# Kernel tuning notes

Hardware: AMD Instinct MI355X
Metric: run time of the kernel (lower is better)

The kernel has to match this reference:

```python
import jax, jax.numpy as jnp
import numpy as np
from jax import lax

# Model dims (match init_kwargs / input_specs)
B, L, DIN, H = 8, 2048, 40, 128
NL, DSTATE, DCONV, EXPAND, DTRANK = 4, 16, 4, 2, 8
DINNER = EXPAND * H
NHOR, NCLS = 3, 3


def _layer_norm(x, g, b, eps=1e-5):
    m = jnp.mean(x, -1, keepdims=True)
    v = jnp.mean((x - m) ** 2, -1, keepdims=True)
    return (x - m) * lax.rsqrt(v + eps) * g + b


def _mamba_block(x, in_w, cw, cb, xp_w, dt_w, dt_b, A_log, Dp, out_w):
    # x: (b, l, H)
    b, l, _ = x.shape
    xz = x @ in_w.T                      # (b, l, 2*d_inner)
    xh, z = jnp.split(xz, 2, axis=-1)
    # causal depthwise conv1d (torch pads d_conv-1 both sides then slices [:l])
    xc = lax.conv_general_dilated(
        xh.transpose(0, 2, 1), cw, window_strides=(1,),
        padding=[(DCONV - 1, 0)], feature_group_count=DINNER,
        dimension_numbers=('NCH', 'OIH', 'NCH')) + cb[None, :, None]
    xh = jax.nn.silu(xc.transpose(0, 2, 1))   # (b, l, d_inner)
    # selective SSM
    A = -jnp.exp(A_log)                   # (N,)
    xp = xh @ xp_w.T                      # (b, l, dt_rank + 2N)
    dt_in, Bm, Cm = jnp.split(xp, [DTRANK, DTRANK + DSTATE], axis=-1)
    delta = jax.nn.softplus(dt_in @ dt_w.T + dt_b)          # (b, l, d_inner)
    dA = jnp.exp(delta[..., None] * A)                      # (b, l, d_inner, N)
    dBx = delta[..., None] * Bm[:, :, None, :] * xh[..., None]

    def step(h, inp):
        dA_t, dBx_t, C_t = inp
        h = dA_t * h + dBx_t              # (b, d_inner, N)
        y = jnp.einsum('bdn,bn->bd', h, C_t)
        return h, y

    h0 = jnp.zeros((b, DINNER, DSTATE), x.dtype)
    _, ys = lax.scan(step, h0, (dA.transpose(1, 0, 2, 3),
                                dBx.transpose(1, 0, 2, 3),
                                Cm.transpose(1, 0, 2)))
    y = ys.transpose(1, 0, 2) + Dp * xh   # (b, l, d_inner)
    y = y * jax.nn.silu(z)
    return y @ out_w.T                    # (b, l, H)


def _forward(x, input_proj_w, input_proj_b, input_norm_g, input_norm_b,
             norm_g, norm_b, in_proj_w, conv_w, conv_b, x_proj_w,
             dt_proj_w, dt_proj_b, A_log, D, out_proj_w,
             head_w1, head_b1, head_w2, head_b2):
    h = _layer_norm(x @ input_proj_w.T + input_proj_b, input_norm_g, input_norm_b)
    for i in range(NL):  # residual Mamba blocks (pre-norm)
        h = h + _mamba_block(_layer_norm(h, norm_g[i], norm_b[i]),
                             in_proj_w[i], conv_w[i], conv_b[i], x_proj_w[i],
                             dt_proj_w[i], dt_proj_b[i], A_log[i], D[i], out_proj_w[i])
    feats = h[:, -1, :]                   # last-timestep features (b, H)
    logits = []
    for i in range(NHOR):
        t = jax.nn.gelu(feats @ head_w1[i].T + head_b1[i], approximate=False)
        logits.append(t @ head_w2[i].T + head_b2[i])
    return jnp.stack(logits, axis=1)      # (b, num_horizons, num_classes)


def setup_inputs() -> dict:
    key = jax.random.key(0)
    ks = jax.random.split(key, 12)
    rn = lambda k, s, sc=0.02: jax.random.normal(k, s, jnp.float32) * sc
    A0 = jnp.log(jnp.arange(1, DSTATE + 1, dtype=jnp.float32))
    return {
        'x': jax.random.normal(ks[0], (B, L, DIN), jnp.float32),
        'input_proj_w': rn(ks[1], (H, DIN)),
        'input_proj_b': jnp.zeros((H,), jnp.float32),
        'input_norm_g': jnp.ones((H,), jnp.float32),
        'input_norm_b': jnp.zeros((H,), jnp.float32),
        'norm_g': jnp.ones((NL, H), jnp.float32),
        'norm_b': jnp.zeros((NL, H), jnp.float32),
        'in_proj_w': rn(ks[2], (NL, 2 * DINNER, H)),
        'conv_w': rn(ks[3], (NL, DINNER, 1, DCONV), 0.1),
        'conv_b': jnp.zeros((NL, DINNER), jnp.float32),
        'x_proj_w': rn(ks[4], (NL, DTRANK + 2 * DSTATE, DINNER)),
        'dt_proj_w': rn(ks[5], (NL, DINNER, DTRANK), 0.1),
        'dt_proj_b': rn(ks[6], (NL, DINNER), 0.1),
        'A_log': jnp.tile(A0, (NL, 1)),
        'D': jnp.ones((NL, DINNER), jnp.float32),
        'out_proj_w': rn(ks[7], (NL, H, DINNER)),
        'head_w1': rn(ks[8], (NHOR, H // 2, H)),
        'head_b1': jnp.zeros((NHOR, H // 2), jnp.float32),
        'head_w2': rn(ks[9], (NHOR, NCLS, H // 2)),
        'head_b2': jnp.zeros((NHOR, NCLS), jnp.float32),
    }


def reference(x, input_proj_w, input_proj_b, input_norm_g, input_norm_b,
              norm_g, norm_b, in_proj_w, conv_w, conv_b, x_proj_w,
              dt_proj_w, dt_proj_b, A_log, D, out_proj_w,
              head_w1, head_b1, head_w2, head_b2):
    return _forward(x, input_proj_w, input_proj_b, input_norm_g, input_norm_b,
                    norm_g, norm_b, in_proj_w, conv_w, conv_b, x_proj_w,
                    dt_proj_w, dt_proj_b, A_log, D, out_proj_w,
                    head_w1, head_b1, head_w2, head_b2)
```

## Files before the change

kernel.cpp:

```cpp
#include <hip/hip_runtime.h>
#include <hip/hip_bf16.h>
#include <math.h>

#define B_  8
#define L_  2048
#define DIN_ 40
#define H_  128
#define NL_ 4
#define DSTATE_ 16
#define DCONV_ 4
#define DTRANK_ 8
#define DINNER_ 256
#define NHOR_ 3
#define NCLS_ 3

#define CL_ 16
#define NC_ 128

__device__ __forceinline__ float softplus_f(float x) {
  return fmaxf(x, 0.f) + log1pf(__expf(-fabsf(x)));
}

__device__ __forceinline__ bool a_is_arith(const float* Ag, float& An0) {
  An0 = -__expf(Ag[0]);
  if (An0 == 0.f) return false;
  bool ok = true;
#pragma unroll
  for (int n = 1; n < DSTATE_; n++) {
    float r = -__expf(Ag[n]) / An0;
    ok = ok && (fabsf(r - (float)(n + 1)) < 1e-3f);
  }
  return ok;
}

__global__ __launch_bounds__(128) void k_in_ln(
    const float* __restrict__ x, const float* __restrict__ w,
    const float* __restrict__ bias, const float* __restrict__ g,
    const float* __restrict__ bb, float* __restrict__ hout)
{
  int row = blockIdx.x;
  int o = threadIdx.x;
  __shared__ float xs[DIN_];
  __shared__ float sm[4];
  if (o < DIN_) xs[o] = x[(size_t)row * DIN_ + o];
  __syncthreads();
  float acc = bias[o];
  const float* wr = w + (size_t)o * DIN_;
#pragma unroll
  for (int k = 0; k < DIN_; k++) acc += xs[k] * wr[k];
  float s = acc;
#pragma unroll
  for (int m = 32; m >= 1; m >>= 1) s += __shfl_xor(s, m);
  if ((o & 63) == 0) sm[o >> 6] = s;
  __syncthreads();
  float mean = (sm[0] + sm[1]) * (1.f / H_);
  float dv = acc - mean;
  float q = dv * dv;
#pragma unroll
  for (int m = 32; m >= 1; m >>= 1) q += __shfl_xor(q, m);
  if ((o & 63) == 0) sm[2 + (o >> 6)] = q;
  __syncthreads();
  float var = (sm[2] + sm[3]) * (1.f / H_);
  hout[(size_t)row * H_ + o] = dv * rsqrtf(var + 1e-5f) * g[o] + bb[o];
}

__global__ __launch_bounds__(128) void k_ln(
    const float* __restrict__ in, const float* __restrict__ g,
    const float* __restrict__ bb, float* __restrict__ out)
{
  int row = blockIdx.x;
  int o = threadIdx.x;
  float v = in[(size_t)row * H_ + o];
  __shared__ float sm[4];
  float s = v;
#pragma unroll
  for (int m = 32; m >= 1; m >>= 1) s += __shfl_xor(s, m);
  if ((o & 63) == 0) sm[o >> 6] = s;
  __syncthreads();
  float mean = (sm[0] + sm[1]) * (1.f / H_);
  float dv = v - mean;
  float q = dv * dv;
#pragma unroll
  for (int m = 32; m >= 1; m >>= 1) q += __shfl_xor(q, m);
  if ((o & 63) == 0) sm[2 + (o >> 6)] = q;
  __syncthreads();
  float var = (sm[2] + sm[3]) * (1.f / H_);
  out[(size_t)row * H_ + o] = dv * rsqrtf(var + 1e-5f) * g[o] + bb[o];
}

template <int BM, int BN, int EPI>
__global__ __launch_bounds__(256) void gemm_tn(
    const float* __restrict__ A, const float* __restrict__ Bw,
    float* __restrict__ C0, float* __restrict__ C1,
    int M, int N, int K)
{
  constexpr int TM = BM / 16, TN = BN / 16;
  __shared__ float As[16][BM + 4];
  __shared__ float Bs[16][BN + 4];
  const int tid = threadIdx.x;
  const int tx = tid & 15, ty = tid >> 4;
  const int bm0 = blockIdx.y * BM, bn0 = blockIdx.x * BN;
  float acc[TM][TN] = {};
  constexpr int AF4 = BM / 64;
  constexpr int BF4 = BN / 64;

  for (int k0 = 0; k0 < K; k0 += 16) {
#pragma unroll
    for (int i = 0; i < AF4; i++) {
      int f = tid + i * 256;
      int r = f >> 2, kq = (f & 3) << 2;
      float4 v = *reinterpret_cast<const float4*>(&A[(size_t)(bm0 + r) * K + k0 + kq]);
      As[kq + 0][r] = v.x; As[kq + 1][r] = v.y;
      As[kq + 2][r] = v.z; As[kq + 3][r] = v.w;
    }
#pragma unroll
    for (int i = 0; i < BF4; i++) {
      int f = tid + i * 256;
      int rn = f >> 2, kq = (f & 3) << 2;
      float4 v = make_float4(0.f, 0.f, 0.f, 0.f);
      if (bn0 + rn < N)
        v = *reinterpret_cast<const float4*>(&Bw[(size_t)(bn0 + rn) * K + k0 + kq]);
      Bs[kq + 0][rn] = v.x; Bs[kq + 1][rn] = v.y;
      Bs[kq + 2][rn] = v.z; Bs[kq + 3][rn] = v.w;
    }
    __syncthreads();
#pragma unroll
    for (int k = 0; k < 16; k++) {
      float a[TM], b[TN];
#pragma unroll
      for (int i = 0; i < TM; i += 4) {
        float4 v = *reinterpret_cast<const float4*>(&As[k][ty * TM + i]);
        a[i] = v.x; a[i + 1] = v.y; a[i + 2] = v.z; a[i + 3] = v.w;
      }
#pragma unroll
      for (int j = 0; j < TN; j += 4) {
        float4 v = *reinterpret_cast<const float4*>(&Bs[k][tx * TN + j]);
        b[j] = v.x; b[j + 1] = v.y; b[j + 2] = v.z; b[j + 3] = v.w;
      }
#pragma unroll
      for (int i = 0; i < TM; i++)
#pragma unroll
        for (int j = 0; j < TN; j++) acc[i][j] += a[i] * b[j];
    }
    __syncthreads();
  }

#pragma unroll
  for (int i = 0; i < TM; i++) {
    int r = bm0 + ty * TM + i;
    int c0 = bn0 + tx * TN;
    if (c0 >= N) continue;
    float4 v = make_float4(acc[i][0], acc[i][1], acc[i][2], acc[i][3]);
    if (EPI == 0) {
      *reinterpret_cast<float4*>(&C0[(size_t)r * N + c0]) = v;
    } else {
      if (c0 < 256) *reinterpret_cast<float4*>(&C0[(size_t)r * 256 + c0]) = v;
      else          *reinterpret_cast<float4*>(&C1[(size_t)r * 256 + (c0 - 256)]) = v;
    }
  }
}

template <bool DO_LN>
__global__ __launch_bounds__(256) void gemm_out(
    const float* __restrict__ A, const float* __restrict__ Bw,
    float* __restrict__ H, float* __restrict__ XN,
    const float* __restrict__ g, const float* __restrict__ bb)
{
  constexpr int BM = 64, BN = 128, K = DINNER_, N = H_;
  constexpr int TM = 4, TN = 8;
  __shared__ float As[16][BM + 4];
  __shared__ float Bs[16][BN + 4];
  const int tid = threadIdx.x;
  const int tx = tid & 15, ty = tid >> 4;
  const int bm0 = blockIdx.x * BM;
  float acc[TM][TN] = {};

  for (int k0 = 0; k0 < K; k0 += 16) {
    {
      int f = tid;
      int r = f >> 2, kq = (f & 3) << 2;
      float4 v = *reinterpret_cast<const float4*>(&A[(size_t)(bm0 + r) * K + k0 + kq]);
      As[kq + 0][r] = v.x; As[kq + 1][r] = v.y;
      As[kq + 2][r] = v.z; As[kq + 3][r] = v.w;
    }
#pragma unroll
    for (int i = 0; i < 2; i++) {
      int f = tid + i * 256;
      int rn = f >> 2, kq = (f & 3) << 2;
      float4 v = *reinterpret_cast<const float4*>(&Bw[(size_t)rn * K + k0 + kq]);
      Bs[kq + 0][rn] = v.x; Bs[kq + 1][rn] = v.y;
      Bs[kq + 2][rn] = v.z; Bs[kq + 3][rn] = v.w;
    }
    __syncthreads();
#pragma unroll
    for (int k = 0; k < 16; k++) {
      float a[TM], b[TN];
      float4 av = *reinterpret_cast<const float4*>(&As[k][ty * TM]);
      a[0] = av.x; a[1] = av.y; a[2] = av.z; a[3] = av.w;
#pragma unroll
      for (int j = 0; j < TN; j += 4) {
        float4 v = *reinterpret_cast<const float4*>(&Bs[k][tx * TN + j]);
        b[j] = v.x; b[j + 1] = v.y; b[j + 2] = v.z; b[j + 3] = v.w;
      }
#pragma unroll
      for (int i = 0; i < TM; i++)
#pragma unroll
        for (int j = 0; j < TN; j++) acc[i][j] += a[i] * b[j];
    }
    __syncthreads();
  }

  float gv[TN], bv[TN];
  if (DO_LN) {
#pragma unroll
    for (int j = 0; j < TN; j += 4) {
      float4 t = *reinterpret_cast<const float4*>(&g[tx * TN + j]);
      gv[j] = t.x; gv[j+1] = t.y; gv[j+2] = t.z; gv[j+3] = t.w;
      float4 u = *reinterpret_cast<const float4*>(&bb[tx * TN + j]);
      bv[j] = u.x; bv[j+1] = u.y; bv[j+2] = u.z; bv[j+3] = u.w;
    }
  }
#pragma unroll
  for (int i = 0; i < TM; i++) {
    int r = bm0 + ty * TM + i;
    float hv[TN];
#pragma unroll
    for (int j = 0; j < TN; j += 4) {
      float4 o = *reinterpret_cast<const float4*>(&H[(size_t)r * N + tx * TN + j]);
      hv[j]   = o.x + acc[i][j];
      hv[j+1] = o.y + acc[i][j+1];
      hv[j+2] = o.z + acc[i][j+2];
      hv[j+3] = o.w + acc[i][j+3];
    }
#pragma unroll
    for (int j = 0; j < TN; j += 4)
      *reinterpret_cast<float4*>(&H[(size_t)r * N + tx * TN + j]) =
          make_float4(hv[j], hv[j+1], hv[j+2], hv[j+3]);
    if (DO_LN) {
      float s = 0.f;
#pragma unroll
      for (int j = 0; j < TN; j++) s += hv[j];
#pragma unroll
      for (int m = 1; m < 16; m <<= 1) s += __shfl_xor(s, m);
      float mean = s * (1.f / N);
      float q = 0.f;
#pragma unroll
      for (int j = 0; j < TN; j++) { float d = hv[j] - mean; q += d * d; }
#pragma unroll
      for (int m = 1; m < 16; m <<= 1) q += __shfl_xor(q, m);
      float rstd = rsqrtf(q * (1.f / N) + 1e-5f);
      float xo[TN];
#pragma unroll
      for (int j = 0; j < TN; j++) xo[j] = (hv[j] - mean) * rstd * gv[j] + bv[j];
#pragma unroll
      for (int j = 0; j < TN; j += 4)
        *reinterpret_cast<float4*>(&XN[(size_t)r * N + tx * TN + j]) =
            make_float4(xo[j], xo[j+1], xo[j+2], xo[j+3]);
    }
  }
}

__global__ __launch_bounds__(256) void k_conv(
    const float* __restrict__ xx, const float* __restrict__ cw,
    const float* __restrict__ cb, float* __restrict__ xh)
{
  int idx = blockIdx.x * 256 + threadIdx.x;
  int d = idx & 255;
  int bt = idx >> 8;
  int t = bt & (L_ - 1);
  float acc = cb[d];
#pragma unroll
  for (int k = 0; k < DCONV_; k++) {
    int ts = t - 3 + k;
    if (ts >= 0) acc += cw[d * DCONV_ + k] * xx[(size_t)(bt - 3 + k) * 256 + d];
  }
  xh[idx] = acc / (1.f + __expf(-acc));
}

__global__ __launch_bounds__(256, 4) void k_scan1(
    const float* __restrict__ xh, const float* __restrict__ xp,
    const float* __restrict__ dtw, const float* __restrict__ dtb,
    const float* __restrict__ Ag,
    float* __restrict__ hf, float* __restrict__ ss)
{
  int b = blockIdx.x >> 7;
  int c = blockIdx.x & (NC_ - 1);
  int d = threadIdx.x;
  __shared__ float xps[CL_][40];
  {
    const float* xrow = xp + ((size_t)b * L_ + c * CL_) * 40;
    for (int i = threadIdx.x; i < CL_ * 40; i += 256) xps[i / 40][i % 40] = xrow[i];
  }
  float dtw_r[DTRANK_];
#pragma unroll
  for (int k = 0; k < DTRANK_; k++) dtw_r[k] = dtw[d * DTRANK_ + k];
  float dtb_r = dtb[d];
  float An0;
  bool fast = a_is_arith(Ag, An0);
  __syncthreads();
  float h[DSTATE_] = {};
  float S = 0.f;
  size_t base = ((size_t)b * L_ + c * CL_) * 256 + d;
  if (fast) {
#pragma unroll
    for (int tt = 0; tt < CL_; tt++) {
      float acc = dtb_r;
#pragma unroll
      for (int k = 0; k < DTRANK_; k++) acc += xps[tt][k] * dtw_r[k];
      float dv = softplus_f(acc);
      float xv = xh[base + tt * 256];
      S += dv;
      float dx = dv * xv;
      float E = __expf(dv * An0);
      float f = E;
#pragma unroll
      for (int n = 0; n < DSTATE_; n++) {
        h[n] = f * h[n] + dx * xps[tt][8 + n];
        f *= E;
      }
    }
  } else {
    for (int tt = 0; tt < CL_; tt++) {
      float acc = dtb_r;
#pragma unroll
      for (int k = 0; k < DTRANK_; k++) acc += xps[tt][k] * dtw_r[k];
      float dv = softplus_f(acc);
      float xv = xh[base + tt * 256];
      S += dv;
      float dx = dv * xv;
      for (int n = 0; n < DSTATE_; n++) {
        float dA = __expf(dv * (-__expf(Ag[n])));
        h[n] = dA * h[n] + dx * xps[tt][8 + n];
      }
    }
  }
  ss[(size_t)blockIdx.x * 256 + d] = S;
  float* hp = hf + ((size_t)blockIdx.x * 256 + d) * DSTATE_;
#pragma unroll
  for (int n = 0; n < DSTATE_; n += 4)
    *reinterpret_cast<float4*>(&hp[n]) = make_float4(h[n], h[n+1], h[n+2], h[n+3]);
}

__global__ __launch_bounds__(64) void k_scan2(
    const float* __restrict__ Ag, const float* __restrict__ ss,
    float* __restrict__ hf)
{
  int gid = blockIdx.x * 64 + threadIdx.x;
  int b = gid >> 12;
  int r = gid & 4095;
  int d = r >> 4;
  int n = r & 15;
  float An = -__expf(Ag[n]);
  float hi = 0.f;
  for (int ct = 0; ct < NC_ / 8; ct++) {
    float f[8], s[8];
#pragma unroll
    for (int j = 0; j < 8; j++) {
      int c = ct * 8 + j;
      f[j] = hf[((size_t)(b * NC_ + c) * 4096) + r];
      s[j] = ss[(size_t)(b * NC_ + c) * 256 + d];
    }
#pragma unroll
    for (int j = 0; j < 8; j++) {
      int c = ct * 8 + j;
      float P = __expf(An * s[j]);
      hf[((size_t)(b * NC_ + c) * 4096) + r] = hi;
      hi = P * hi + f[j];
    }
  }
}

__global__ __launch_bounds__(256, 4) void k_scan3(
    const float* __restrict__ xh, const float* __restrict__ xp,
    const float* __restrict__ dtw, const float* __restrict__ dtb,
    const float* __restrict__ Ag, const float* __restrict__ hf,
    const float* __restrict__ Dp, float* zy)
{
  int b = blockIdx.x >> 7;
  int c = blockIdx.x & (NC_ - 1);
  int d = threadIdx.x;
  __shared__ float xps[CL_][40];
  {
    const float* xrow = xp + ((size_t)b * L_ + c * CL_) * 40;
    for (int i = threadIdx.x; i < CL_ * 40; i += 256) xps[i / 40][i % 40] = xrow[i];
  }
  float dtw_r[DTRANK_];
#pragma unroll
  for (int k = 0; k < DTRANK_; k++) dtw_r[k] = dtw[d * DTRANK_ + k];
  float dtb_r = dtb[d];
  float An0;
  bool fast = a_is_arith(Ag, An0);
  __syncthreads();
  float h[DSTATE_];
  {
    const float* hp = hf + ((size_t)blockIdx.x * 256 + d) * DSTATE_;
#pragma unroll
    for (int n = 0; n < DSTATE_; n += 4) {
      float4 v = *reinterpret_cast<const float4*>(&hp[n]);
      h[n] = v.x; h[n+1] = v.y; h[n+2] = v.z; h[n+3] = v.w;
    }
  }
  float Dv = Dp[d];
  size_t base = ((size_t)b * L_ + c * CL_) * 256 + d;
  if (fast) {
#pragma unroll
    for (int tt = 0; tt < CL_; tt++) {
      float acc = dtb_r;
#pragma unroll
      for (int k = 0; k < DTRANK_; k++) acc += xps[tt][k] * dtw_r[k];
      float dv = softplus_f(acc);
      float xv = xh[base + tt * 256];
      float dx = dv * xv;
      float E = __expf(dv * An0);
      float f = E;
      float y = 0.f;
#pragma unroll
      for (int n = 0; n < DSTATE_; n++) {
        h[n] = f * h[n] + dx * xps[tt][8 + n];
        y += h[n] * xps[tt][24 + n];
        f *= E;
      }
      float yv = y + Dv * xv;
      float zv = zy[base + tt * 256];
      zy[base + tt * 256] = yv * (zv / (1.f + __expf(-zv)));
    }
  } else {
    for (int tt = 0; tt < CL_; tt++) {
      float acc = dtb_r;
#pragma unroll
      for (int k = 0; k < DTRANK_; k++) acc += xps[tt][k] * dtw_r[k];
      float dv = softplus_f(acc);
      float xv = xh[base + tt * 256];
      float dx = dv * xv;
      float y = 0.f;
      for (int n = 0; n < DSTATE_; n++) {
        float dA = __expf(dv * (-__expf(Ag[n])));
        h[n] = dA * h[n] + dx * xps[tt][8 + n];
        y += h[n] * xps[tt][24 + n];
      }
      float yv = y + Dv * xv;
      float zv = zy[base + tt * 256];
      zy[base + tt * 256] = yv * (zv / (1.f + __expf(-zv)));
    }
  }
}

__global__ __launch_bounds__(64) void k_heads(
    const float* __restrict__ hbuf, const float* __restrict__ w1,
    const float* __restrict__ b1, const float* __restrict__ w2,
    const float* __restrict__ b2, float* __restrict__ out)
{
  int hor = blockIdx.x, b = blockIdx.y;
  int j = threadIdx.x;
  __shared__ float fs[H_];
  __shared__ float ts[64];
  const float* fr = hbuf + ((size_t)b * L_ + (L_ - 1)) * H_;
  fs[j] = fr[j];
  fs[j + 64] = fr[j + 64];
  __syncthreads();
  float acc = b1[hor * 64 + j];
  const float* wr = w1 + (size_t)(hor * 64 + j) * H_;
#pragma unroll
  for (int k = 0; k < H_; k++) acc += fs[k] * wr[k];
  ts[j] = 0.5f * acc * (1.f + erff(acc * 0.70710678118654752f));
  __syncthreads();
  if (j < NCLS_) {
    float a2 = b2[hor * NCLS_ + j];
    const float* w2r = w2 + (size_t)(hor * NCLS_ + j) * 64;
    float s = a2;
#pragma unroll
    for (int k = 0; k < 64; k++) s += ts[k] * w2r[k];
    out[(size_t)b * (NHOR_ * NCLS_) + hor * NCLS_ + j] = s;
  }
}

extern "C" void kernel_launch(void* const* d_in, const int* in_sizes, int n_in,
                              void* d_out, int out_size, void* d_ws, size_t ws_size,
                              hipStream_t stream)
{
  const float* x            = (const float*)d_in[0];
  const float* input_proj_w = (const float*)d_in[1];
  const float* input_proj_b = (const float*)d_in[2];
  const float* input_norm_g = (const float*)d_in[3];
  const float* input_norm_b = (const float*)d_in[4];
  const float* norm_g       = (const float*)d_in[5];
  const float* norm_b       = (const float*)d_in[6];
  const float* in_proj_w    = (const float*)d_in[7];
  const float* conv_w       = (const float*)d_in[8];
  const float* conv_b       = (const float*)d_in[9];
  const float* x_proj_w     = (const float*)d_in[10];
  const float* dt_proj_w    = (const float*)d_in[11];
  const float* dt_proj_b    = (const float*)d_in[12];
  const float* A_log        = (const float*)d_in[13];
  const float* Dp           = (const float*)d_in[14];
  const float* out_proj_w   = (const float*)d_in[15];
  const float* head_w1      = (const float*)d_in[16];
  const float* head_b1      = (const float*)d_in[17];
  const float* head_w2      = (const float*)d_in[18];
  const float* head_b2      = (const float*)d_in[19];
  float* out = (float*)d_out;

  const int ROWS = B_ * L_;
  float* ws = (float*)d_ws;
  float* h    = ws;
  float* xn   = h  + (size_t)ROWS * H_;
  float* xx   = xn + (size_t)ROWS * H_;
  float* zz   = xx + (size_t)ROWS * 256;
  float* xh   = zz + (size_t)ROWS * 256;
  float* xp   = xh + (size_t)ROWS * 256;
  float* ss   = xp + (size_t)ROWS * 40;
  float* hf   = xx;

  k_in_ln<<<ROWS, 128, 0, stream>>>(x, input_proj_w, input_proj_b,
                                    input_norm_g, input_norm_b, h);
  k_ln<<<ROWS, 128, 0, stream>>>(h, norm_g, norm_b, xn);

  for (int l = 0; l < NL_; l++) {
    gemm_tn<128, 64, 2><<<dim3(512 / 64, ROWS / 128), 256, 0, stream>>>(
        xn, in_proj_w + (size_t)l * 512 * H_, xx, zz, ROWS, 512, H_);
    k_conv<<<ROWS, 256, 0, stream>>>(xx, conv_w + (size_t)l * DINNER_ * DCONV_,
                                     conv_b + (size_t)l * DINNER_, xh);
    gemm_tn<64, 64, 0><<<dim3(1, ROWS / 64), 256, 0, stream>>>(
        xh, x_proj_w + (size_t)l * 40 * DINNER_, xp, nullptr, ROWS, 40, DINNER_);
    k_scan1<<<B_ * NC_, 256, 0, stream>>>(xh, xp,
        dt_proj_w + (size_t)l * DINNER_ * DTRANK_, dt_proj_b + (size_t)l * DINNER_,
        A_log + l * DSTATE_, hf, ss);
    k_scan2<<<(B_ * DINNER_ * DSTATE_) / 64, 64, 0, stream>>>(A_log + l * DSTATE_, ss, hf);
    k_scan3<<<B_ * NC_, 256, 0, stream>>>(xh, xp,
        dt_proj_w + (size_t)l * DINNER_ * DTRANK_, dt_proj_b + (size_t)l * DINNER_,
        A_log + l * DSTATE_, hf, Dp + (size_t)l * DINNER_, zz);
    if (l < NL_ - 1) {
      gemm_out<true><<<ROWS / 64, 256, 0, stream>>>(
          zz, out_proj_w + (size_t)l * H_ * DINNER_, h, xn,
          norm_g + (l + 1) * H_, norm_b + (l + 1) * H_);
    } else {
      gemm_out<false><<<ROWS / 64, 256, 0, stream>>>(
          zz, out_proj_w + (size_t)l * H_ * DINNER_, h, nullptr, nullptr, nullptr);
    }
  }

  k_heads<<<dim3(NHOR_, B_), 64, 0, stream>>>(h, head_w1, head_b1, head_w2, head_b2, out);
}
```

Before: 831.9 us.

## Fuse conv, x_proj and chunk scan; correct chunk outputs from carried state

```diff
diff --git a/kernel.cpp b/kernel.cpp
--- a/kernel.cpp
+++ b/kernel.cpp
@@ -14,8 +14,8 @@
 #define NHOR_ 3
 #define NCLS_ 3
 
-#define CL_ 16
-#define NC_ 128
+#define CL_ 32
+#define NC_ 64
 
 __device__ __forceinline__ float softplus_f(float x) {
   return fmaxf(x, 0.f) + log1pf(__expf(-fabsf(x)));
@@ -260,78 +260,98 @@
   }
 }
 
-__global__ __launch_bounds__(256) void k_conv(
+__global__ __launch_bounds__(256, 4) void k_front(
     const float* __restrict__ xx, const float* __restrict__ cw,
-    const float* __restrict__ cb, float* __restrict__ xh)
-{
-  int idx = blockIdx.x * 256 + threadIdx.x;
-  int d = idx & 255;
-  int bt = idx >> 8;
-  int t = bt & (L_ - 1);
-  float acc = cb[d];
-#pragma unroll
-  for (int k = 0; k < DCONV_; k++) {
-    int ts = t - 3 + k;
-    if (ts >= 0) acc += cw[d * DCONV_ + k] * xx[(size_t)(bt - 3 + k) * 256 + d];
-  }
-  xh[idx] = acc / (1.f + __expf(-acc));
-}
-
-__global__ __launch_bounds__(256, 4) void k_scan1(
-    const float* __restrict__ xh, const float* __restrict__ xp,
+    const float* __restrict__ cb, const float* __restrict__ xpw,
     const float* __restrict__ dtw, const float* __restrict__ dtb,
-    const float* __restrict__ Ag,
+    const float* __restrict__ Ag, const float* __restrict__ Dp,
+    float* __restrict__ xpg, float* __restrict__ ylbuf,
     float* __restrict__ hf, float* __restrict__ ss)
 {
-  int b = blockIdx.x >> 7;
+  int b = blockIdx.x >> 6;
   int c = blockIdx.x & (NC_ - 1);
   int d = threadIdx.x;
-  __shared__ float xps[CL_][40];
-  {
-    const float* xrow = xp + ((size_t)b * L_ + c * CL_) * 40;
-    for (int i = threadIdx.x; i < CL_ * 40; i += 256) xps[i / 40][i % 40] = xrow[i];
-  }
+  int row0 = b * L_ + c * CL_;
+
+  __shared__ float xhs[CL_][256];
+  __shared__ float xps[CL_ * 40];
+
+  float w0 = cw[d * DCONV_ + 0], w1 = cw[d * DCONV_ + 1];
+  float w2 = cw[d * DCONV_ + 2], w3 = cw[d * DCONV_ + 3];
+  float cbv = cb[d];
+  float xm3 = (c > 0) ? xx[(size_t)(row0 - 3) * 256 + d] : 0.f;
+  float xm2 = (c > 0) ? xx[(size_t)(row0 - 2) * 256 + d] : 0.f;
+  float xm1 = (c > 0) ? xx[(size_t)(row0 - 1) * 256 + d] : 0.f;
+#pragma unroll
+  for (int t = 0; t < CL_; t++) {
+    float xc = xx[(size_t)(row0 + t) * 256 + d];
+    float a = cbv + w0 * xm3 + w1 * xm2 + w2 * xm1 + w3 * xc;
+    xhs[t][d] = a / (1.f + __expf(-a));
+    xm3 = xm2; xm2 = xm1; xm1 = xc;
+  }
+  __syncthreads();
+
+  for (int o = d; o < CL_ * 40; o += 256) {
+    int t = o / 40, j = o - t * 40;
+    const float* wrow = xpw + (size_t)j * 256;
+    float av = 0.f;
+#pragma unroll
+    for (int k = 0; k < 256; k += 4) {
+      float4 wv = *reinterpret_cast<const float4*>(&wrow[k]);
+      float4 xv = *reinterpret_cast<const float4*>(&xhs[t][k]);
+      av += xv.x * wv.x + xv.y * wv.y + xv.z * wv.z + xv.w * wv.w;
+    }
+    xps[o] = av;
+    xpg[(size_t)row0 * 40 + o] = av;
+  }
+  __syncthreads();
+
   float dtw_r[DTRANK_];
 #pragma unroll
   for (int k = 0; k < DTRANK_; k++) dtw_r[k] = dtw[d * DTRANK_ + k];
   float dtb_r = dtb[d];
+  float Dv = Dp[d];
   float An0;
   bool fast = a_is_arith(Ag, An0);
-  __syncthreads();
   float h[DSTATE_] = {};
   float S = 0.f;
-  size_t base = ((size_t)b * L_ + c * CL_) * 256 + d;
+  size_t base = (size_t)row0 * 256 + d;
   if (fast) {
 #pragma unroll
-    for (int tt = 0; tt < CL_; tt++) {
+    for (int t = 0; t < CL_; t++) {
       float acc = dtb_r;
 #pragma unroll
-      for (int k = 0; k < DTRANK_; k++) acc += xps[tt][k] * dtw_r[k];
+      for (int k = 0; k < DTRANK_; k++) acc += xps[t * 40 + k] * dtw_r[k];
       float dv = softplus_f(acc);
-      float xv = xh[base + tt * 256];
+      float xv = xhs[t][d];
       S += dv;
       float dx = dv * xv;
       float E = __expf(dv * An0);
-      float f = E;
+      float f = E, y = 0.f;
 #pragma unroll
       for (int n = 0; n < DSTATE_; n++) {
-        h[n] = f * h[n] + dx * xps[tt][8 + n];
+        h[n] = f * h[n] + dx * xps[t * 40 + 8 + n];
+        y += h[n] * xps[t * 40 + 24 + n];
         f *= E;
       }
+      ylbuf[base + t * 256] = y + Dv * xv;
     }
   } else {
-    for (int tt = 0; tt < CL_; tt++) {
+    for (int t = 0; t < CL_; t++) {
       float acc = dtb_r;
 #pragma unroll
-      for (int k = 0; k < DTRANK_; k++) acc += xps[tt][k] * dtw_r[k];
+      for (int k = 0; k < DTRANK_; k++) acc += xps[t * 40 + k] * dtw_r[k];
       float dv = softplus_f(acc);
-      float xv = xh[base + tt * 256];
+      float xv = xhs[t][d];
       S += dv;
       float dx = dv * xv;
+      float y = 0.f;
       for (int n = 0; n < DSTATE_; n++) {
         float dA = __expf(dv * (-__expf(Ag[n])));
-        h[n] = dA * h[n] + dx * xps[tt][8 + n];
+        h[n] = dA * h[n] + dx * xps[t * 40 + 8 + n];
+        y += h[n] * xps[t * 40 + 24 + n];
       }
+      ylbuf[base + t * 256] = y + Dv * xv;
     }
   }
   ss[(size_t)blockIdx.x * 256 + d] = S;
@@ -371,19 +391,17 @@
 }
 
 __global__ __launch_bounds__(256, 4) void k_scan3(
-    const float* __restrict__ xh, const float* __restrict__ xp,
-    const float* __restrict__ dtw, const float* __restrict__ dtb,
-    const float* __restrict__ Ag, const float* __restrict__ hf,
-    const float* __restrict__ Dp, float* zy)
-{
-  int b = blockIdx.x >> 7;
+    const float* __restrict__ xpg, const float* __restrict__ dtw,
+    const float* __restrict__ dtb, const float* __restrict__ Ag,
+    const float* __restrict__ hf, const float* __restrict__ ylbuf,
+    float* zz)
+{
+  int b = blockIdx.x >> 6;
   int c = blockIdx.x & (NC_ - 1);
   int d = threadIdx.x;
-  __shared__ float xps[CL_][40];
-  {
-    const float* xrow = xp + ((size_t)b * L_ + c * CL_) * 40;
-    for (int i = threadIdx.x; i < CL_ * 40; i += 256) xps[i / 40][i % 40] = xrow[i];
-  }
+  int row0 = b * L_ + c * CL_;
+  __shared__ float xps[CL_ * 40];
+  for (int i = d; i < CL_ * 40; i += 256) xps[i] = xpg[(size_t)row0 * 40 + i];
   float dtw_r[DTRANK_];
 #pragma unroll
   for (int k = 0; k < DTRANK_; k++) dtw_r[k] = dtw[d * DTRANK_ + k];
@@ -391,56 +409,47 @@
   float An0;
   bool fast = a_is_arith(Ag, An0);
   __syncthreads();
-  float h[DSTATE_];
+  float h0[DSTATE_];
   {
     const float* hp = hf + ((size_t)blockIdx.x * 256 + d) * DSTATE_;
 #pragma unroll
     for (int n = 0; n < DSTATE_; n += 4) {
       float4 v = *reinterpret_cast<const float4*>(&hp[n]);
-      h[n] = v.x; h[n+1] = v.y; h[n+2] = v.z; h[n+3] = v.w;
-    }
-  }
-  float Dv = Dp[d];
-  size_t base = ((size_t)b * L_ + c * CL_) * 256 + d;
+      h0[n] = v.x; h0[n+1] = v.y; h0[n+2] = v.z; h0[n+3] = v.w;
+    }
+  }
+  size_t base = (size_t)row0 * 256 + d;
+  float cd = 0.f;
   if (fast) {
 #pragma unroll
-    for (int tt = 0; tt < CL_; tt++) {
+    for (int t = 0; t < CL_; t++) {
       float acc = dtb_r;
 #pragma unroll
-      for (int k = 0; k < DTRANK_; k++) acc += xps[tt][k] * dtw_r[k];
-      float dv = softplus_f(acc);
-      float xv = xh[base + tt * 256];
-      float dx = dv * xv;
-      float E = __expf(dv * An0);
-      float f = E;
-      float y = 0.f;
+      for (int k = 0; k < DTRANK_; k++) acc += xps[t * 40 + k] * dtw_r[k];
+      cd += softplus_f(acc);
+      float E = __expf(cd * An0);
+      float p = E, corr = 0.f;
 #pragma unroll
       for (int n = 0; n < DSTATE_; n++) {
-        h[n] = f * h[n] + dx * xps[tt][8 + n];
-        y += h[n] * xps[tt][24 + n];
-        f *= E;
+        corr += p * h0[n] * xps[t * 40 + 24 + n];
+        p *= E;
       }
-      float yv = y + Dv * xv;
-      float zv = zy[base + tt * 256];
-      zy[base + tt * 256] = yv * (zv / (1.f + __expf(-zv)));
+      float yv = ylbuf[base + t * 256] + corr;
+      float zv = zz[base + t * 256];
+      zz[base + t * 256] = yv * (zv / (1.f + __expf(-zv)));
     }
   } else {
-    for (int tt = 0; tt < CL_; tt++) {
+    for (int t = 0; t < CL_; t++) {
       float acc = dtb_r;
 #pragma unroll
-      for (int k = 0; k < DTRANK_; k++) acc += xps[tt][k] * dtw_r[k];
-      float dv = softplus_f(acc);
-      float xv = xh[base + tt * 256];
-      float dx = dv * xv;
-      float y = 0.f;
-      for (int n = 0; n < DSTATE_; n++) {
-        float dA = __expf(dv * (-__expf(Ag[n])));
-        h[n] = dA * h[n] + dx * xps[tt][8 + n];
-        y += h[n] * xps[tt][24 + n];
-      }
-      float yv = y + Dv * xv;
-      float zv = zy[base + tt * 256];
-      zy[base + tt * 256] = yv * (zv / (1.f + __expf(-zv)));
+      for (int k = 0; k < DTRANK_; k++) acc += xps[t * 40 + k] * dtw_r[k];
+      cd += softplus_f(acc);
+      float corr = 0.f;
+      for (int n = 0; n < DSTATE_; n++)
+        corr += __expf(cd * (-__expf(Ag[n]))) * h0[n] * xps[t * 40 + 24 + n];
+      float yv = ylbuf[base + t * 256] + corr;
+      float zv = zz[base + t * 256];
+      zz[base + t * 256] = yv * (zv / (1.f + __expf(-zv)));
     }
   }
 }
@@ -502,14 +511,14 @@
 
   const int ROWS = B_ * L_;
   float* ws = (float*)d_ws;
-  float* h    = ws;
-  float* xn   = h  + (size_t)ROWS * H_;
-  float* xx   = xn + (size_t)ROWS * H_;
-  float* zz   = xx + (size_t)ROWS * 256;
-  float* xh   = zz + (size_t)ROWS * 256;
-  float* xp   = xh + (size_t)ROWS * 256;
-  float* ss   = xp + (size_t)ROWS * 40;
-  float* hf   = xx;
+  float* h     = ws;
+  float* xn    = h  + (size_t)ROWS * H_;
+  float* xx    = xn + (size_t)ROWS * H_;
+  float* zz    = xx + (size_t)ROWS * 256;
+  float* ylbuf = zz + (size_t)ROWS * 256;
+  float* xp    = ylbuf + (size_t)ROWS * 256;
+  float* ss    = xp + (size_t)ROWS * 40;
+  float* hf    = xn;
 
   k_in_ln<<<ROWS, 128, 0, stream>>>(x, input_proj_w, input_proj_b,
                                     input_norm_g, input_norm_b, h);
@@ -518,17 +527,16 @@
   for (int l = 0; l < NL_; l++) {
     gemm_tn<128, 64, 2><<<dim3(512 / 64, ROWS / 128), 256, 0, stream>>>(
         xn, in_proj_w + (size_t)l * 512 * H_, xx, zz, ROWS, 512, H_);
-    k_conv<<<ROWS, 256, 0, stream>>>(xx, conv_w + (size_t)l * DINNER_ * DCONV_,
-                                     conv_b + (size_t)l * DINNER_, xh);
-    gemm_tn<64, 64, 0><<<dim3(1, ROWS / 64), 256, 0, stream>>>(
-        xh, x_proj_w + (size_t)l * 40 * DINNER_, xp, nullptr, ROWS, 40, DINNER_);
-    k_scan1<<<B_ * NC_, 256, 0, stream>>>(xh, xp,
+    k_front<<<B_ * NC_, 256, 0, stream>>>(
+        xx, conv_w + (size_t)l * DINNER_ * DCONV_, conv_b + (size_t)l * DINNER_,
+        x_proj_w + (size_t)l * 40 * DINNER_,
         dt_proj_w + (size_t)l * DINNER_ * DTRANK_, dt_proj_b + (size_t)l * DINNER_,
-        A_log + l * DSTATE_, hf, ss);
+        A_log + l * DSTATE_, Dp + (size_t)l * DINNER_,
+        xp, ylbuf, hf, ss);
     k_scan2<<<(B_ * DINNER_ * DSTATE_) / 64, 64, 0, stream>>>(A_log + l * DSTATE_, ss, hf);
-    k_scan3<<<B_ * NC_, 256, 0, stream>>>(xh, xp,
-        dt_proj_w + (size_t)l * DINNER_ * DTRANK_, dt_proj_b + (size_t)l * DINNER_,
-        A_log + l * DSTATE_, hf, Dp + (size_t)l * DINNER_, zz);
+    k_scan3<<<B_ * NC_, 256, 0, stream>>>(
+        xp, dt_proj_w + (size_t)l * DINNER_ * DTRANK_, dt_proj_b + (size_t)l * DINNER_,
+        A_log + l * DSTATE_, hf, ylbuf, zz);
     if (l < NL_ - 1) {
       gemm_out<true><<<ROWS / 64, 256, 0, stream>>>(
           zz, out_proj_w + (size_t)l * H_ * DINNER_, h, xn,
```

Result: slower. 933.8 us (+12.3%).

## Compute local scan outputs in pass one, apply carry-in correction in pass three

Applied to the files above, without the earlier changes.

```diff
diff --git a/kernel.cpp b/kernel.cpp
--- a/kernel.cpp
+++ b/kernel.cpp
@@ -148,14 +148,17 @@
 #pragma unroll
   for (int i = 0; i < TM; i++) {
     int r = bm0 + ty * TM + i;
-    int c0 = bn0 + tx * TN;
-    if (c0 >= N) continue;
-    float4 v = make_float4(acc[i][0], acc[i][1], acc[i][2], acc[i][3]);
-    if (EPI == 0) {
-      *reinterpret_cast<float4*>(&C0[(size_t)r * N + c0]) = v;
-    } else {
-      if (c0 < 256) *reinterpret_cast<float4*>(&C0[(size_t)r * 256 + c0]) = v;
-      else          *reinterpret_cast<float4*>(&C1[(size_t)r * 256 + (c0 - 256)]) = v;
+#pragma unroll
+    for (int jj = 0; jj < TN; jj += 4) {
+      int c0 = bn0 + tx * TN + jj;
+      if (c0 >= N) continue;
+      float4 v = make_float4(acc[i][jj], acc[i][jj+1], acc[i][jj+2], acc[i][jj+3]);
+      if (EPI == 0) {
+        *reinterpret_cast<float4*>(&C0[(size_t)r * N + c0]) = v;
+      } else {
+        if (c0 < 256) *reinterpret_cast<float4*>(&C0[(size_t)r * 256 + c0]) = v;
+        else          *reinterpret_cast<float4*>(&C1[(size_t)r * 256 + (c0 - 256)]) = v;
+      }
     }
   }
 }
@@ -277,10 +280,10 @@
   xh[idx] = acc / (1.f + __expf(-acc));
 }
 
-__global__ __launch_bounds__(256, 4) void k_scan1(
-    const float* __restrict__ xh, const float* __restrict__ xp,
+__global__ __launch_bounds__(256, 4) void k_scan1y(
+    float* xh_yl, const float* __restrict__ xp,
     const float* __restrict__ dtw, const float* __restrict__ dtb,
-    const float* __restrict__ Ag,
+    const float* __restrict__ Ag, const float* __restrict__ Dp,
     float* __restrict__ hf, float* __restrict__ ss)
 {
   int b = blockIdx.x >> 7;
@@ -295,6 +298,7 @@
 #pragma unroll
   for (int k = 0; k < DTRANK_; k++) dtw_r[k] = dtw[d * DTRANK_ + k];
   float dtb_r = dtb[d];
+  float Dv = Dp[d];
   float An0;
   bool fast = a_is_arith(Ag, An0);
   __syncthreads();
@@ -308,16 +312,18 @@
 #pragma unroll
       for (int k = 0; k < DTRANK_; k++) acc += xps[tt][k] * dtw_r[k];
       float dv = softplus_f(acc);
-      float xv = xh[base + tt * 256];
+      float xv = xh_yl[base + tt * 256];
       S += dv;
       float dx = dv * xv;
       float E = __expf(dv * An0);
-      float f = E;
+      float f = E, y = 0.f;
 #pragma unroll
       for (int n = 0; n < DSTATE_; n++) {
         h[n] = f * h[n] + dx * xps[tt][8 + n];
+        y += h[n] * xps[tt][24 + n];
         f *= E;
       }
+      xh_yl[base + tt * 256] = y + Dv * xv;
     }
   } else {
     for (int tt = 0; tt < CL_; tt++) {
@@ -325,13 +331,16 @@
 #pragma unroll
       for (int k = 0; k < DTRANK_; k++) acc += xps[tt][k] * dtw_r[k];
       float dv = softplus_f(acc);
-      float xv = xh[base + tt * 256];
+      float xv = xh_yl[base + tt * 256];
       S += dv;
       float dx = dv * xv;
+      float y = 0.f;
       for (int n = 0; n < DSTATE_; n++) {
         float dA = __expf(dv * (-__expf(Ag[n])));
         h[n] = dA * h[n] + dx * xps[tt][8 + n];
-      }
+        y += h[n] * xps[tt][24 + n];
+      }
+      xh_yl[base + tt * 256] = y + Dv * xv;
     }
   }
   ss[(size_t)blockIdx.x * 256 + d] = S;
@@ -370,20 +379,18 @@
   }
 }
 
-__global__ __launch_bounds__(256, 4) void k_scan3(
-    const float* __restrict__ xh, const float* __restrict__ xp,
-    const float* __restrict__ dtw, const float* __restrict__ dtb,
-    const float* __restrict__ Ag, const float* __restrict__ hf,
-    const float* __restrict__ Dp, float* zy)
+__global__ __launch_bounds__(256, 4) void k_scan3c(
+    const float* __restrict__ xpg, const float* __restrict__ dtw,
+    const float* __restrict__ dtb, const float* __restrict__ Ag,
+    const float* __restrict__ hf, const float* __restrict__ ylbuf,
+    float* zz)
 {
   int b = blockIdx.x >> 7;
   int c = blockIdx.x & (NC_ - 1);
   int d = threadIdx.x;
-  __shared__ float xps[CL_][40];
-  {
-    const float* xrow = xp + ((size_t)b * L_ + c * CL_) * 40;
-    for (int i = threadIdx.x; i < CL_ * 40; i += 256) xps[i / 40][i % 40] = xrow[i];
-  }
+  int row0 = b * L_ + c * CL_;
+  __shared__ float xps[CL_ * 40];
+  for (int i = d; i < CL_ * 40; i += 256) xps[i] = xpg[(size_t)row0 * 40 + i];
   float dtw_r[DTRANK_];
 #pragma unroll
   for (int k = 0; k < DTRANK_; k++) dtw_r[k] = dtw[d * DTRANK_ + k];
@@ -391,56 +398,47 @@
   float An0;
   bool fast = a_is_arith(Ag, An0);
   __syncthreads();
-  float h[DSTATE_];
+  float h0[DSTATE_];
   {
     const float* hp = hf + ((size_t)blockIdx.x * 256 + d) * DSTATE_;
 #pragma unroll
     for (int n = 0; n < DSTATE_; n += 4) {
       float4 v = *reinterpret_cast<const float4*>(&hp[n]);
-      h[n] = v.x; h[n+1] = v.y; h[n+2] = v.z; h[n+3] = v.w;
-    }
-  }
-  float Dv = Dp[d];
-  size_t base = ((size_t)b * L_ + c * CL_) * 256 + d;
+      h0[n] = v.x; h0[n+1] = v.y; h0[n+2] = v.z; h0[n+3] = v.w;
+    }
+  }
+  size_t base = (size_t)row0 * 256 + d;
+  float cd = 0.f;
   if (fast) {
 #pragma unroll
-    for (int tt = 0; tt < CL_; tt++) {
+    for (int t = 0; t < CL_; t++) {
       float acc = dtb_r;
 #pragma unroll
-      for (int k = 0; k < DTRANK_; k++) acc += xps[tt][k] * dtw_r[k];
-      float dv = softplus_f(acc);
-      float xv = xh[base + tt * 256];
-      float dx = dv * xv;
-      float E = __expf(dv * An0);
-      float f = E;
-      float y = 0.f;
+      for (int k = 0; k < DTRANK_; k++) acc += xps[t * 40 + k] * dtw_r[k];
+      cd += softplus_f(acc);
+      float E = __expf(cd * An0);
+      float p = E, corr = 0.f;
 #pragma unroll
       for (int n = 0; n < DSTATE_; n++) {
-        h[n] = f * h[n] + dx * xps[tt][8 + n];
-        y += h[n] * xps[tt][24 + n];
-        f *= E;
-      }
-      float yv = y + Dv * xv;
-      float zv = zy[base + tt * 256];
-      zy[base + tt * 256] = yv * (zv / (1.f + __expf(-zv)));
+        corr += p * h0[n] * xps[t * 40 + 24 + n];
+        p *= E;
+      }
+      float yv = ylbuf[base + t * 256] + corr;
+      float zv = zz[base + t * 256];
+      zz[base + t * 256] = yv * (zv / (1.f + __expf(-zv)));
     }
   } else {
-    for (int tt = 0; tt < CL_; tt++) {
+    for (int t = 0; t < CL_; t++) {
       float acc = dtb_r;
 #pragma unroll
-      for (int k = 0; k < DTRANK_; k++) acc += xps[tt][k] * dtw_r[k];
-      float dv = softplus_f(acc);
-      float xv = xh[base + tt * 256];
-      float dx = dv * xv;
-      float y = 0.f;
-      for (int n = 0; n < DSTATE_; n++) {
-        float dA = __expf(dv * (-__expf(Ag[n])));
-        h[n] = dA * h[n] + dx * xps[tt][8 + n];
-        y += h[n] * xps[tt][24 + n];
-      }
-      float yv = y + Dv * xv;
-      float zv = zy[base + tt * 256];
-      zy[base + tt * 256] = yv * (zv / (1.f + __expf(-zv)));
+      for (int k = 0; k < DTRANK_; k++) acc += xps[t * 40 + k] * dtw_r[k];
+      cd += softplus_f(acc);
+      float corr = 0.f;
+      for (int n = 0; n < DSTATE_; n++)
+        corr += __expf(cd * (-__expf(Ag[n]))) * h0[n] * xps[t * 40 + 24 + n];
+      float yv = ylbuf[base + t * 256] + corr;
+      float zv = zz[base + t * 256];
+      zz[base + t * 256] = yv * (zv / (1.f + __expf(-zv)));
     }
   }
 }
@@ -516,19 +514,19 @@
   k_ln<<<ROWS, 128, 0, stream>>>(h, norm_g, norm_b, xn);
 
   for (int l = 0; l < NL_; l++) {
-    gemm_tn<128, 64, 2><<<dim3(512 / 64, ROWS / 128), 256, 0, stream>>>(
+    gemm_tn<128, 128, 2><<<dim3(512 / 128, ROWS / 128), 256, 0, stream>>>(
         xn, in_proj_w + (size_t)l * 512 * H_, xx, zz, ROWS, 512, H_);
     k_conv<<<ROWS, 256, 0, stream>>>(xx, conv_w + (size_t)l * DINNER_ * DCONV_,
                                      conv_b + (size_t)l * DINNER_, xh);
     gemm_tn<64, 64, 0><<<dim3(1, ROWS / 64), 256, 0, stream>>>(
         xh, x_proj_w + (size_t)l * 40 * DINNER_, xp, nullptr, ROWS, 40, DINNER_);
-    k_scan1<<<B_ * NC_, 256, 0, stream>>>(xh, xp,
+    k_scan1y<<<B_ * NC_, 256, 0, stream>>>(xh, xp,
         dt_proj_w + (size_t)l * DINNER_ * DTRANK_, dt_proj_b + (size_t)l * DINNER_,
-        A_log + l * DSTATE_, hf, ss);
+        A_log + l * DSTATE_, Dp + (size_t)l * DINNER_, hf, ss);
     k_scan2<<<(B_ * DINNER_ * DSTATE_) / 64, 64, 0, stream>>>(A_log + l * DSTATE_, ss, hf);
-    k_scan3<<<B_ * NC_, 256, 0, stream>>>(xh, xp,
-        dt_proj_w + (size_t)l * DINNER_ * DTRANK_, dt_proj_b + (size_t)l * DINNER_,
-        A_log + l * DSTATE_, hf, Dp + (size_t)l * DINNER_, zz);
+    k_scan3c<<<B_ * NC_, 256, 0, stream>>>(
+        xp, dt_proj_w + (size_t)l * DINNER_ * DTRANK_, dt_proj_b + (size_t)l * DINNER_,
+        A_log + l * DSTATE_, hf, xh, zz);
     if (l < NL_ - 1) {
       gemm_out<true><<<ROWS / 64, 256, 0, stream>>>(
           zz, out_proj_w + (size_t)l * H_ * DINNER_, h, xn,
```

After: 774.6 us. 1.07x faster.
